# Performance work log

Measured on AMD Instinct MI355X. Metric: run time of the kernel, lower is better.

## Reference

```python
import jax, jax.numpy as jnp
import numpy as np
import math

PI = math.pi
PATCH_SIZE = 32
NUM_BINS = 36
EPS = 1e-8


def setup_inputs() -> dict:
    key = jax.random.key(0)
    patch = jax.random.normal(key, (65536, 1, PATCH_SIZE, PATCH_SIZE), dtype=jnp.float32)
    return {"patch": patch}


def reference(patch):
    B = patch.shape[0]
    dt = patch.dtype
    # kornia SpatialGradient('sobel', 1): L1-normalized sobel kernels, replicate padding
    kx = jnp.array([[-1.0, 0.0, 1.0], [-2.0, 0.0, 2.0], [-1.0, 0.0, 1.0]], dtype=dt) / 8.0
    ky = kx.T
    kernel = jnp.stack([kx, ky])[:, None]  # [2,1,3,3] OIHW
    padded = jnp.pad(patch, ((0, 0), (0, 0), (1, 1), (1, 1)), mode="edge")
    grads = jax.lax.conv_general_dilated(
        padded, kernel, window_strides=(1, 1), padding="VALID",
        dimension_numbers=("NCHW", "OIHW", "NCHW"))  # [B,2,H,W]
    gx, gy = grads[:, 0], grads[:, 1]
    mag = jnp.sqrt(gx * gx + gy * gy + EPS)
    ori = jnp.arctan2(gy, gx + EPS) + 2.0 * PI
    o_big = float(NUM_BINS) * (ori + PI) / (2.0 * PI)
    bo0 = jnp.floor(o_big)
    wo1 = o_big - bo0
    b0 = (bo0 % NUM_BINS).astype(jnp.int32)
    b1 = (b0 + 1) % NUM_BINS
    w0 = (1.0 - wo1) * mag
    w1 = wo1 * mag
    npix = PATCH_SIZE * PATCH_SIZE
    # soft histogram via scatter-add; adaptive_avg_pool2d(1,1) == mean over pixels
    def histo(b0f, b1f, w0f, w1f):
        return jnp.zeros(NUM_BINS, dtype=dt).at[b0f].add(w0f).at[b1f].add(w1f)
    hist = jax.vmap(histo)(b0.reshape(B, -1), b1.reshape(B, -1),
                           w0.reshape(B, -1), w1.reshape(B, -1)) / npix
    # circular conv1d with fixed kernel [0.33, 0.34, 0.33]
    sm = 0.33 * jnp.roll(hist, 1, axis=-1) + 0.34 * hist + 0.33 * jnp.roll(hist, -1, axis=-1)
    indices = jnp.argmax(sm, axis=-1)
    angle = -(2.0 * PI * indices.astype(dt) / float(NUM_BINS) - PI)
    return angle
```

## Files before the change

### kernel.cpp

```cpp
#include <hip/hip_runtime.h>
#include <math.h>

#pragma clang fp contract(off)

#define NBINS 36
#define PS 32

__device__ __forceinline__ float atan2_np(float fy, float fx)
{
    const double aT0  =  3.33333333333329318027e-01;
    const double aT1  = -1.99999999998764832476e-01;
    const double aT2  =  1.42857142725034663711e-01;
    const double aT3  = -1.11111104054623557880e-01;
    const double aT4  =  9.09088713343650656196e-02;
    const double aT5  = -7.69187620504482999495e-02;
    const double aT6  =  6.66107313738753120669e-02;
    const double aT7  = -5.83357013379057348645e-02;
    const double aT8  =  4.97687799461593236017e-02;
    const double aT9  = -3.65315727442169155270e-02;
    const double aT10 =  1.62858201153657823623e-02;

    float axf = fabsf(fx), ayf = fabsf(fy);
    float uf = fmaxf(axf, ayf), vf = fminf(axf, ayf);
    bool g1 = vf >= 0.41421356f * uf;

    double u = (double)uf, v = (double)vf;
    double c      = g1 ? 1.0 : 0.0;
    double atc_hi = g1 ? 7.85398163397448278999e-01 : 0.0;
    double atc_lo = g1 ? 3.06161699786838301793e-17 : 0.0;

    double num = fma(-c, u, v);
    double den = fma(c, v, u);

    double r0 = __builtin_amdgcn_rcp(den);
    r0 = fma(fma(-den, r0, 1.0), r0, r0);
    r0 = fma(fma(-den, r0, 1.0), r0, r0);
    double q0 = num * r0;
    double xq = fma(fma(-den, q0, num), r0, q0);

    double z = xq * xq;
    double w = z * z;
    double s1_ = z * fma(w, fma(w, fma(w, fma(w, fma(w, aT10, aT8), aT6), aT4), aT2), aT0);
    double s2_ = w * fma(w, fma(w, fma(w, fma(w, aT9, aT7), aT5), aT3), aT1);
    double p   = xq * (s1_ + s2_);
    double res = atc_hi - ((p - atc_lo) - xq);

    double res2 = (1.57079632679489655800e+00 - res) + 6.12323399573676603587e-17;
    res = (ayf > axf) ? res2 : res;
    double res3 = (3.14159265358979311600e+00 - res) + 1.22464679914735317723e-16;
    res = (fx < 0.0f) ? res3 : res;
    res = copysign(res, (double)fy);
    return (float)res;
}

__device__ __forceinline__ float dpp_prev(float x) {
    int i = __builtin_bit_cast(int, x);
    int r = __builtin_amdgcn_update_dpp(i, i, 0x111, 0xf, 0xf, false);
    return __builtin_bit_cast(float, r);
}
__device__ __forceinline__ float dpp_next(float x) {
    int i = __builtin_bit_cast(int, x);
    int r = __builtin_amdgcn_update_dpp(i, i, 0x101, 0xf, 0xf, false);
    return __builtin_bit_cast(float, r);
}

__global__ __launch_bounds__(256)
void patch_orient_kernel(const float* __restrict__ patches, float* __restrict__ out)
{
    __shared__ __align__(16) float tile[PS][PS];
    __shared__ unsigned bm[PS][NBINS];
    __shared__ unsigned short pref[PS][NBINS];
    __shared__ unsigned short cnt[NBINS];
    __shared__ unsigned short start[NBINS];
    __shared__ __align__(16) float s0[1024];
    __shared__ __align__(16) float s1[1024];
    __shared__ float hsm[NBINS];

    const int t = threadIdx.x;
    const int b = blockIdx.x;
    const float* p = patches + (size_t)b * (PS * PS);

    #pragma unroll
    for (int i = t; i < PS * NBINS; i += 256) ((unsigned*)bm)[i] = 0u;

    ((float4*)tile)[t] = ((const float4*)p)[t];
    __syncthreads();

    const int row = t >> 3;
    const int cb  = (t & 7) << 2;
    const int rm  = (row == 0)  ? 0  : row - 1;
    const int rp  = (row == 31) ? 31 : row + 1;

    float win[3][6];
    {
        const int rows[3] = {rm, row, rp};
        #pragma unroll
        for (int r = 0; r < 3; ++r) {
            float4 v = *((const float4*)&tile[rows[r]][cb]);
            float lf = dpp_prev(v.w);
            float rt = dpp_next(v.x);
            win[r][0] = (cb == 0)  ? v.x : lf;
            win[r][1] = v.x; win[r][2] = v.y; win[r][3] = v.z; win[r][4] = v.w;
            win[r][5] = (cb == 28) ? v.w : rt;
        }
    }

    const float TWO_PI = 6.2831853071795864769f;
    const float PI_F   = 3.14159265358979323846f;
    const float INV2PI = 0.15915493667125701904f;

    float w0r[4], w1r[4];
    int   binr[4];

    #pragma unroll
    for (int i = 0; i < 4; ++i) {
        float A = win[0][i], B = win[0][i + 1], C = win[0][i + 2];
        float D = win[1][i],                    F = win[1][i + 2];
        float G = win[2][i], H = win[2][i + 1], I = win[2][i + 2];

        float gx = -0.125f * A;
        gx += 0.125f  * C;
        gx += -0.25f  * D;
        gx += 0.25f   * F;
        gx += -0.125f * G;
        gx += 0.125f  * I;

        float gy = -0.125f * A;
        gy += -0.25f  * B;
        gy += -0.125f * C;
        gy += 0.125f  * G;
        gy += 0.25f   * H;
        gy += 0.125f  * I;

        float m1 = gx * gx;
        float m2 = gy * gy;
        float s  = m1 + m2;
        s = s + 1e-8f;
        float mag = sqrtf(s);

        float gxe = gx + 1e-8f;
        float at  = atan2_np(gy, gxe);
        float ori = at + TWO_PI;
        float xn  = 36.0f * (ori + PI_F);
        float q1m = xn * INV2PI;
        float obig = fmaf(fmaf(-TWO_PI, q1m, xn), INV2PI, q1m);
        float bo0  = floorf(obig);
        float wo1  = obig - bo0;

        int bi0 = (int)bo0 - 36;
        if (bi0 < 0)   bi0 += 36;
        if (bi0 >= 36) bi0 -= 36;

        w0r[i]  = (1.0f - wo1) * mag;
        w1r[i]  = wo1 * mag;
        binr[i] = bi0;
        atomicOr(&bm[row][bi0], 1u << (cb + i));
    }
    __syncthreads();

    if (t < 64) {
        unsigned run = 0;
        if (t < NBINS) {
            #pragma unroll 1
            for (int w = 0; w < PS; ++w) {
                pref[w][t] = (unsigned short)run;
                run += __popc(bm[w][t]);
            }
            cnt[t] = (unsigned short)run;
        }
        unsigned v = run;
        #pragma unroll
        for (int d = 1; d < 64; d <<= 1) {
            unsigned o = (unsigned)__shfl_up((int)v, d);
            if (t >= d) v += o;
        }
        if (t < NBINS) start[t] = (unsigned short)(v - run);
    }
    __syncthreads();

    #pragma unroll
    for (int i = 0; i < 4; ++i) {
        const int bi = binr[i];
        const unsigned lowmask = (1u << (cb + i)) - 1u;
        const int pos = (int)start[bi] + (int)pref[row][bi]
                      + __popc(bm[row][bi] & lowmask);
        s0[pos] = w0r[i];
        s1[pos] = w1r[i];
    }
    __syncthreads();

    if (t < NBINS) {
        float acc = 0.0f;
        {
            int i = start[t], en = i + cnt[t];
            for (; i + 1 < en; i += 2) { acc += s0[i]; acc += s0[i + 1]; }
            if (i < en) acc += s0[i];
        }
        {
            int t2 = (t == 0) ? NBINS - 1 : t - 1;
            int i = start[t2], en = i + cnt[t2];
            for (; i + 1 < en; i += 2) { acc += s1[i]; acc += s1[i + 1]; }
            if (i < en) acc += s1[i];
        }
        hsm[t] = acc * (1.0f / 1024.0f);
    }
    __syncthreads();

    if (t < 64) {
        float val = -1.0f;
        int   idx = t;
        if (t < NBINS) {
            int im_ = (t == 0)         ? NBINS - 1 : t - 1;
            int ip_ = (t == NBINS - 1) ? 0         : t + 1;
            float q0 = 0.33f * hsm[im_];
            float q1 = 0.34f * hsm[t];
            float q2 = 0.33f * hsm[t == NBINS - 1 ? 0 : t + 1] * 0.0f + 0.33f * hsm[ip_];
            val = (q0 + q1) + q2;
        }
        #pragma unroll
        for (int d = 1; d < 64; d <<= 1) {
            float ov = __shfl_xor(val, d);
            int   oi = __shfl_xor(idx, d);
            if (ov > val || (ov == val && oi < idx)) { val = ov; idx = oi; }
        }
        if (t == 0) {
            float t1 = TWO_PI * (float)idx;
            float t2 = t1 / 36.0f;
            float t3 = t2 - PI_F;
            out[b] = -t3;
        }
    }
}

extern "C" void kernel_launch(void* const* d_in, const int* in_sizes, int n_in,
                              void* d_out, int out_size, void* d_ws, size_t ws_size,
                              hipStream_t stream) {
    const float* patch = (const float*)d_in[0];
    float* out = (float*)d_out;
    const int B = in_sizes[0] / (PS * PS);
    patch_orient_kernel<<<B, 256, 0, stream>>>(patch, out);
}
```

Before: 521.6 us.

## Trim atan2 Newton step, swizzle shared tile, unroll prefix and sum loops

Drops one double-precision Newton refinement of the reciprocal in atan2 and fuses the polynomial multiply with the low-part subtraction into one FMA. Stores the patch tile in shared memory with an XOR swizzle to reduce bank conflicts on the row window loads. Unrolls the per-bin prefix-count loop by eight and the histogram summation loops by four, and removes a redundant zero-multiplied term in the smoothing step. The reduced Newton step and the added FMA rounding change atan2 precision slightly, which can move values near bin boundaries.

```diff
diff --git a/kernel.cpp b/kernel.cpp
--- a/kernel.cpp
+++ b/kernel.cpp
@@ -34,7 +34,6 @@
 
     double r0 = __builtin_amdgcn_rcp(den);
     r0 = fma(fma(-den, r0, 1.0), r0, r0);
-    r0 = fma(fma(-den, r0, 1.0), r0, r0);
     double q0 = num * r0;
     double xq = fma(fma(-den, q0, num), r0, q0);
 
@@ -42,8 +41,8 @@
     double w = z * z;
     double s1_ = z * fma(w, fma(w, fma(w, fma(w, fma(w, aT10, aT8), aT6), aT4), aT2), aT0);
     double s2_ = w * fma(w, fma(w, fma(w, fma(w, aT9, aT7), aT5), aT3), aT1);
-    double p   = xq * (s1_ + s2_);
-    double res = atc_hi - ((p - atc_lo) - xq);
+    double T   = fma(xq, s1_ + s2_, -atc_lo);
+    double res = atc_hi - (T - xq);
 
     double res2 = (1.57079632679489655800e+00 - res) + 6.12323399573676603587e-17;
     res = (ayf > axf) ? res2 : res;
@@ -67,7 +66,7 @@
 __global__ __launch_bounds__(256)
 void patch_orient_kernel(const float* __restrict__ patches, float* __restrict__ out)
 {
-    __shared__ __align__(16) float tile[PS][PS];
+    __shared__ __align__(16) float tile[PS * PS];
     __shared__ unsigned bm[PS][NBINS];
     __shared__ unsigned short pref[PS][NBINS];
     __shared__ unsigned short cnt[NBINS];
@@ -83,20 +82,21 @@
     #pragma unroll
     for (int i = t; i < PS * NBINS; i += 256) ((unsigned*)bm)[i] = 0u;
 
-    ((float4*)tile)[t] = ((const float4*)p)[t];
-    __syncthreads();
-
     const int row = t >> 3;
     const int cb  = (t & 7) << 2;
     const int rm  = (row == 0)  ? 0  : row - 1;
     const int rp  = (row == 31) ? 31 : row + 1;
+
+    *((float4*)&tile[(row << 5) | (cb ^ ((row & 7) << 2))]) = ((const float4*)p)[t];
+    __syncthreads();
 
     float win[3][6];
     {
         const int rows[3] = {rm, row, rp};
         #pragma unroll
         for (int r = 0; r < 3; ++r) {
-            float4 v = *((const float4*)&tile[rows[r]][cb]);
+            const int rr = rows[r];
+            float4 v = *((const float4*)&tile[(rr << 5) | (cb ^ ((rr & 7) << 2))]);
             float lf = dpp_prev(v.w);
             float rt = dpp_next(v.x);
             win[r][0] = (cb == 0)  ? v.x : lf;
@@ -108,6 +108,8 @@
     const float TWO_PI = 6.2831853071795864769f;
     const float PI_F   = 3.14159265358979323846f;
     const float INV2PI = 0.15915493667125701904f;
+
+    const unsigned bitbase = 1u << cb;
 
     float w0r[4], w1r[4];
     int   binr[4];
@@ -154,17 +156,27 @@
         w0r[i]  = (1.0f - wo1) * mag;
         w1r[i]  = wo1 * mag;
         binr[i] = bi0;
-        atomicOr(&bm[row][bi0], 1u << (cb + i));
+        atomicOr(&bm[row][bi0], bitbase << i);
     }
     __syncthreads();
 
     if (t < 64) {
         unsigned run = 0;
         if (t < NBINS) {
-            #pragma unroll 1
-            for (int w = 0; w < PS; ++w) {
-                pref[w][t] = (unsigned short)run;
-                run += __popc(bm[w][t]);
+            #pragma unroll
+            for (int w = 0; w < PS; w += 8) {
+                unsigned m0 = bm[w + 0][t], m1 = bm[w + 1][t];
+                unsigned m2 = bm[w + 2][t], m3 = bm[w + 3][t];
+                unsigned m4 = bm[w + 4][t], m5 = bm[w + 5][t];
+                unsigned m6 = bm[w + 6][t], m7 = bm[w + 7][t];
+                pref[w + 0][t] = (unsigned short)run; run += __popc(m0);
+                pref[w + 1][t] = (unsigned short)run; run += __popc(m1);
+                pref[w + 2][t] = (unsigned short)run; run += __popc(m2);
+                pref[w + 3][t] = (unsigned short)run; run += __popc(m3);
+                pref[w + 4][t] = (unsigned short)run; run += __popc(m4);
+                pref[w + 5][t] = (unsigned short)run; run += __popc(m5);
+                pref[w + 6][t] = (unsigned short)run; run += __popc(m6);
+                pref[w + 7][t] = (unsigned short)run; run += __popc(m7);
             }
             cnt[t] = (unsigned short)run;
         }
@@ -181,7 +193,7 @@
     #pragma unroll
     for (int i = 0; i < 4; ++i) {
         const int bi = binr[i];
-        const unsigned lowmask = (1u << (cb + i)) - 1u;
+        const unsigned lowmask = (bitbase << i) - 1u;
         const int pos = (int)start[bi] + (int)pref[row][bi]
                       + __popc(bm[row][bi] & lowmask);
         s0[pos] = w0r[i];
@@ -193,14 +205,18 @@
         float acc = 0.0f;
         {
             int i = start[t], en = i + cnt[t];
-            for (; i + 1 < en; i += 2) { acc += s0[i]; acc += s0[i + 1]; }
-            if (i < en) acc += s0[i];
+            for (; i + 3 < en; i += 4) {
+                acc += s0[i]; acc += s0[i + 1]; acc += s0[i + 2]; acc += s0[i + 3];
+            }
+            for (; i < en; ++i) acc += s0[i];
         }
         {
             int t2 = (t == 0) ? NBINS - 1 : t - 1;
             int i = start[t2], en = i + cnt[t2];
-            for (; i + 1 < en; i += 2) { acc += s1[i]; acc += s1[i + 1]; }
-            if (i < en) acc += s1[i];
+            for (; i + 3 < en; i += 4) {
+                acc += s1[i]; acc += s1[i + 1]; acc += s1[i + 2]; acc += s1[i + 3];
+            }
+            for (; i < en; ++i) acc += s1[i];
         }
         hsm[t] = acc * (1.0f / 1024.0f);
     }
@@ -214,8 +230,9 @@
             int ip_ = (t == NBINS - 1) ? 0         : t + 1;
             float q0 = 0.33f * hsm[im_];
             float q1 = 0.34f * hsm[t];
-            float q2 = 0.33f * hsm[t == NBINS - 1 ? 0 : t + 1] * 0.0f + 0.33f * hsm[ip_];
-            val = (q0 + q1) + q2;
+            float q2 = 0.33f * hsm[ip_];
+            float val_ = (q0 + q1) + q2;
+            val = val_;
         }
         #pragma unroll
         for (int d = 1; d < 64; d <<= 1) {
```

Result: faster. 492.8 us (-5.5%).
